# Kernel optimization log

Hardware: AMD Instinct MI355X
Metric: run time of the kernel (lower is better)

The kernel has to match this reference:

```python
import jax, jax.numpy as jnp
import numpy as np


def _gcn_conv(x, W, b, src, dst, n_nodes):
    # PyG GCNConv with add_self_loops=True, edge_weight=None (implicit ones),
    # symmetric normalization: D^{-1/2} A_hat D^{-1/2} (X W) + b
    xw = x @ W                                    # [N, H]
    loop = jnp.arange(n_nodes, dtype=src.dtype)
    src_f = jnp.concatenate([src, loop])          # [E+N]
    dst_f = jnp.concatenate([dst, loop])          # [E+N]
    w = jnp.ones(src_f.shape[0], dtype=x.dtype)
    deg = jax.ops.segment_sum(w, dst_f, num_segments=n_nodes)  # in-degree incl. self-loop
    dinv = jnp.where(deg > 0, jax.lax.rsqrt(deg), 0.0)
    norm = dinv[src_f] * dinv[dst_f]              # [E+N]
    msgs = norm[:, None] * xw[src_f]              # [E+N, H]
    out = jax.ops.segment_sum(msgs, dst_f, num_segments=n_nodes)
    return out + b


def setup_inputs() -> dict:
    key = jax.random.key(0)
    k1, k2, k3, k4 = jax.random.split(key, 4)
    N, E, D, H = 100000, 1600000, 256, 128
    x = jax.random.normal(k1, (N, D), dtype=jnp.float32)
    edge_index = jax.random.randint(k2, (2, E), 0, N, dtype=jnp.int64)
    # Glorot-scaled weights
    W1 = jax.random.normal(k3, (D, H), dtype=jnp.float32) * np.sqrt(2.0 / (D + H))
    b1 = jnp.zeros((H,), dtype=jnp.float32)
    W2 = jax.random.normal(k4, (H, 1), dtype=jnp.float32) * np.sqrt(2.0 / (H + 1))
    b2 = jnp.zeros((1,), dtype=jnp.float32)
    return {"x": x, "edge_index": edge_index, "W1": W1, "b1": b1, "W2": W2, "b2": b2}


def reference(x, edge_index, W1, b1, W2, b2):
    n_nodes = x.shape[0]
    src, dst = edge_index[0], edge_index[1]
    h = _gcn_conv(x, W1, b1, src, dst, n_nodes)   # conv1
    h = jax.nn.relu(h)                            # relu; dropout is identity in eval mode
    out = _gcn_conv(h, W2, b2, src, dst, n_nodes) # conv2 -> [N, 1]
    return out.reshape(-1)                        # x.view(-1)
```

## Files before the change

kernel.cpp:

```cpp
#include <hip/hip_runtime.h>
#include <hip/hip_fp16.h>
#include <cstdint>
#include <cstddef>


#define ELLCAP 63
#define BSH 9
#define BNODES (1 << BSH)
#define BPAD 16
#define BCAP 12288

typedef _Float16 half8 __attribute__((ext_vector_type(8)));
typedef _Float16 half2t __attribute__((ext_vector_type(2)));
typedef float floatx4 __attribute__((ext_vector_type(4)));
typedef float floatv4 __attribute__((ext_vector_type(4)));
typedef int intv4 __attribute__((ext_vector_type(4)));
typedef unsigned int uintv4 __attribute__((ext_vector_type(4)));

__global__ __launch_bounds__(256) void prep_k(const float* __restrict__ W1,
                                              _Float16* __restrict__ wz,
                                              _Float16* __restrict__ z1h,
                                              float* __restrict__ z2w,
                                              int* __restrict__ cnt,
                                              int* __restrict__ gcur,
                                              int N, int NB) {
  int b = blockIdx.x, tid = threadIdx.x;
  if (b < 128) {
    int id = b * 256 + tid;
    int j = id & 7, lane = (id >> 3) & 63, nb = (id >> 9) & 7, kb = id >> 12;
    int k = kb * 32 + ((lane >> 4) << 3) + j;
    int n = nb * 16 + (lane & 15);
    wz[id] = (_Float16)W1[k * 128 + n];
  } else if (b == 128) {
    if (tid < 128) z1h[(size_t)N * 128 + tid] = (_Float16)0.f;
    if (tid == 0) { z2w[N] = 0.f; cnt[N] = 0; }
  } else {
    int i = (b - 129) * 256 + tid;
    if (i < NB * BPAD) gcur[i] = 0;
  }
}

__global__ __launch_bounds__(256) void stage_k(int kind, int fb, int g0,
                                               const float* __restrict__ X,
                                               const _Float16* __restrict__ wz,
                                               _Float16* __restrict__ z1h, int N,
                                               const int* __restrict__ src,
                                               const int* __restrict__ dst,
                                               int* __restrict__ gcur,
                                               int* __restrict__ barr,
                                               int* __restrict__ ell,
                                               int* __restrict__ cnt,
                                               int E, int NB) {
  __shared__ char lds_raw[16 * 1024];
  int tid = threadIdx.x;

  if ((int)blockIdx.x < fb) {
    if (kind == 0) {
      int* bc = (int*)lds_raw;
      int* bb = bc + 256;
      for (int i = tid; i < NB; i += 256) bc[i] = 0;
      __syncthreads();
      int base = ((int)blockIdx.x * 256 + tid) * 8;
      int dv[8], sv[8], rv[8], bkv[8];
      int ne = 0;
      if (base + 7 < E) {
        intv4 d0 = __builtin_nontemporal_load((const intv4*)(dst + base));
        intv4 d1 = __builtin_nontemporal_load((const intv4*)(dst + base + 4));
        intv4 s0 = __builtin_nontemporal_load((const intv4*)(src + base));
        intv4 s1 = __builtin_nontemporal_load((const intv4*)(src + base + 4));
        dv[0] = d0[0]; dv[1] = d0[1]; dv[2] = d0[2]; dv[3] = d0[3];
        dv[4] = d1[0]; dv[5] = d1[1]; dv[6] = d1[2]; dv[7] = d1[3];
        sv[0] = s0[0]; sv[1] = s0[1]; sv[2] = s0[2]; sv[3] = s0[3];
        sv[4] = s1[0]; sv[5] = s1[1]; sv[6] = s1[2]; sv[7] = s1[3];
        ne = 8;
      } else {
        for (int e = base; e < E && e < base + 8; ++e) {
          dv[ne] = dst[e]; sv[ne] = src[e]; ++ne;
        }
      }
      for (int i = 0; i < ne; ++i) {
        bkv[i] = dv[i] >> BSH;
        rv[i] = atomicAdd(&bc[bkv[i]], 1);
      }
      __syncthreads();
      for (int i = tid; i < NB; i += 256) {
        int cc = bc[i];
        bb[i] = cc ? atomicAdd(&gcur[i * BPAD], cc) : 0;
      }
      __syncthreads();
      for (int i = 0; i < ne; ++i) {
        int pos = bb[bkv[i]] + rv[i];
        if (pos < BCAP) {
          unsigned dl = (unsigned)(dv[i] & (BNODES - 1));
          barr[(size_t)bkv[i] * BCAP + pos] = (int)((dl << 23) | (unsigned)sv[i]);
        }
      }
    } else {
      int* cl = (int*)lds_raw;
      int bkt = (int)blockIdx.x;
      int lo = bkt << BSH;
      for (int i = tid; i < BNODES; i += 256) cl[i] = 0;
      __syncthreads();
      int cb = min(gcur[bkt * BPAD], BCAP);
      const int* seg = barr + (size_t)bkt * BCAP;
      for (int e = tid; e < cb; e += 256) {
        unsigned v = (unsigned)seg[e];
        int dl = (int)(v >> 23);
        int s = (int)(v & 0x7FFFFFu);
        int p = atomicAdd(&cl[dl], 1);
        if (p < ELLCAP) ell[(size_t)(lo + dl) * 64 + p] = s;
      }
      __syncthreads();
      for (int i = tid; i < BNODES; i += 256) {
        int node = lo + i;
        if (node < N) cnt[node] = cl[i];
      }
    }
    return;
  }

  _Float16* Bl = (_Float16*)lds_raw;
  _Float16* Ol = (_Float16*)lds_raw;

  int wave = tid >> 6, lane = tid & 63;
  int m = lane & 15, q = lane >> 4;
  int row0 = (g0 + (int)blockIdx.x - fb) * 64;
  int row = row0 + wave * 16 + m;

  floatx4 acc[8];
#pragma unroll
  for (int nb = 0; nb < 8; ++nb) acc[nb] = (floatx4)(0.f);

  const uintv4* wsrc = (const uintv4*)wz;
  uintv4* bdst = (uintv4*)Bl;

#pragma unroll
  for (int ph = 0; ph < 4; ++ph) {
    if (ph) __syncthreads();
#pragma unroll
    for (int i = 0; i < 4; ++i) bdst[i * 256 + tid] = wsrc[ph * 1024 + i * 256 + tid];
    __syncthreads();
#pragma unroll
    for (int kk = 0; kk < 2; ++kk) {
      int kb = ph * 2 + kk;
      half8 a;
      if (row < N) {
        const floatv4* ap = (const floatv4*)(X + (size_t)row * 256 + kb * 32 + q * 8);
        floatv4 a0 = __builtin_nontemporal_load(ap);
        floatv4 a1 = __builtin_nontemporal_load(ap + 1);
        a[0] = (_Float16)a0[0]; a[1] = (_Float16)a0[1];
        a[2] = (_Float16)a0[2]; a[3] = (_Float16)a0[3];
        a[4] = (_Float16)a1[0]; a[5] = (_Float16)a1[1];
        a[6] = (_Float16)a1[2]; a[7] = (_Float16)a1[3];
      } else {
#pragma unroll
        for (int j = 0; j < 8; ++j) a[j] = (_Float16)0.f;
      }
#pragma unroll
      for (int nb = 0; nb < 8; ++nb) {
        half8 b = *(const half8*)(Bl + ((size_t)(kk * 8 + nb) * 64 + lane) * 8);
        acc[nb] = __builtin_amdgcn_mfma_f32_16x16x32_f16(a, b, acc[nb], 0, 0, 0);
      }
    }
  }
  __syncthreads();

#pragma unroll
  for (int nb = 0; nb < 8; ++nb) {
    int col = nb * 16 + m;
#pragma unroll
    for (int r = 0; r < 4; ++r) {
      int orow = wave * 16 + q * 4 + r;
      Ol[orow * 128 + col] = (_Float16)acc[nb][r];
    }
  }
  __syncthreads();

  const uintv4* osrc = (const uintv4*)Ol;
  uintv4* gdst = (uintv4*)(z1h + (size_t)row0 * 128);
#pragma unroll
  for (int i = 0; i < 4; ++i) {
    int idx = i * 256 + tid;
    int r = idx >> 4;
    if (row0 + r < N) gdst[idx] = osrc[idx];
  }
}

__global__ __launch_bounds__(256) void agg1_k(const _Float16* __restrict__ z1h,
                                              const int* __restrict__ cnt,
                                              const int* __restrict__ ell,
                                              const float* __restrict__ b1,
                                              const float* __restrict__ W2,
                                              float* __restrict__ z2w, int N) {
  int d = blockIdx.x * 4 + (threadIdx.x >> 6);
  int lane = threadIdx.x & 63;
  if (d >= N) return;
  int cd = cnt[d];
  int c = min(cd, ELLCAP);
  int ct = c + 1;
  int raw = ell[(size_t)d * 64 + lane];
  int up = __shfl_up(raw, 1, 64);
  int idx = (lane == 0) ? d : ((lane < ct) ? up : N);
  float wl = rsqrtf((float)(cnt[idx] + 1));
  float dd = rsqrtf((float)(cd + 1));

  int g = lane >> 4;
  int a8 = (lane & 15) * 8;
  float acc[8];
#pragma unroll
  for (int k = 0; k < 8; ++k) acc[k] = 0.f;

  for (int t = 0; t < ct; t += 8) {
    int s0 = __shfl(idx, t + g, 64);
    float w0 = __shfl(wl, t + g, 64);
    int s1 = __shfl(idx, t + 4 + g, 64);
    float w1 = __shfl(wl, t + 4 + g, 64);
    half8 v0 = *(const half8*)(z1h + (size_t)s0 * 128 + a8);
    half8 v1 = *(const half8*)(z1h + (size_t)s1 * 128 + a8);
#pragma unroll
    for (int k = 0; k < 8; ++k) acc[k] = fmaf(w0, (float)v0[k], acc[k]);
#pragma unroll
    for (int k = 0; k < 8; ++k) acc[k] = fmaf(w1, (float)v1[k], acc[k]);
  }

#pragma unroll
  for (int k = 0; k < 8; ++k) {
    acc[k] += __shfl_xor(acc[k], 16, 64);
    acc[k] += __shfl_xor(acc[k], 32, 64);
  }

  float4 bA = *(const float4*)(b1 + a8);
  float4 bB = *(const float4*)(b1 + a8 + 4);
  float4 wA = *(const float4*)(W2 + a8);
  float4 wB = *(const float4*)(W2 + a8 + 4);
  float dot = fmaxf(fmaf(dd, acc[0], bA.x), 0.f) * wA.x
            + fmaxf(fmaf(dd, acc[1], bA.y), 0.f) * wA.y
            + fmaxf(fmaf(dd, acc[2], bA.z), 0.f) * wA.z
            + fmaxf(fmaf(dd, acc[3], bA.w), 0.f) * wA.w
            + fmaxf(fmaf(dd, acc[4], bB.x), 0.f) * wB.x
            + fmaxf(fmaf(dd, acc[5], bB.y), 0.f) * wB.y
            + fmaxf(fmaf(dd, acc[6], bB.z), 0.f) * wB.z
            + fmaxf(fmaf(dd, acc[7], bB.w), 0.f) * wB.w;
#pragma unroll
  for (int off = 8; off >= 1; off >>= 1) dot += __shfl_xor(dot, off, 64);
  if (lane == 0) z2w[d] = dd * dot;
}

__global__ __launch_bounds__(256) void agg2_k(const float* __restrict__ z2w,
                                              const int* __restrict__ cnt,
                                              const int* __restrict__ ell,
                                              const float* __restrict__ b2,
                                              float* __restrict__ out, int N) {
  int d = blockIdx.x * 4 + (threadIdx.x >> 6);
  int lane = threadIdx.x & 63;
  if (d >= N) return;
  int cd = cnt[d];
  int c = min(cd, ELLCAP);
  int raw = ell[(size_t)d * 64 + lane];
  int idx = (lane < c) ? raw : N;
  float v = z2w[idx];
#pragma unroll
  for (int off = 32; off >= 1; off >>= 1) v += __shfl_xor(v, off, 64);
  if (lane == 0) out[d] = rsqrtf((float)(cd + 1)) * (v + z2w[d]) + b2[0];
}

extern "C" void kernel_launch(void* const* d_in, const int* in_sizes, int n_in,
                              void* d_out, int out_size, void* d_ws, size_t ws_size,
                              hipStream_t stream) {
  (void)n_in; (void)out_size; (void)ws_size;
  const float* x = (const float*)d_in[0];
  const int* edge = (const int*)d_in[1];
  const float* W1 = (const float*)d_in[2];
  const float* b1 = (const float*)d_in[3];
  const float* W2 = (const float*)d_in[4];
  const float* b2 = (const float*)d_in[5];
  float* out = (float*)d_out;

  const int D = 256, H = 128;
  int N = in_sizes[0] / D;
  int E = in_sizes[1] / 2;
  const int* srcp = edge;
  const int* dstp = edge + E;
  int NB = (N + BNODES - 1) >> BSH;

  char* ws = (char*)d_ws;
  size_t off = 0;
  auto alloc = [&](size_t bytes) -> void* {
    void* p = ws + off;
    off += (bytes + 255) & ~(size_t)255;
    return p;
  };
  int* cnt        = (int*)alloc((size_t)(N + 1) * 4);
  float* z2w      = (float*)alloc((size_t)(N + 1) * 4);
  int* ell        = (int*)alloc((size_t)N * 64 * 4);
  _Float16* wz    = (_Float16*)alloc((size_t)32768 * 2);
  _Float16* z1h   = (_Float16*)alloc((size_t)(N + 1) * H * 2);
  int* gcur       = (int*)alloc((size_t)NB * BPAD * 4);
  int* barr       = (int*)alloc((size_t)NB * BCAP * 4);

  int tiles = (N + 63) / 64;
  int fbA = (E + 2047) / 2048;
  int fbB = NB;

  prep_k<<<dim3(129 + (NB * BPAD + 255) / 256), dim3(256), 0, stream>>>(
      W1, wz, z1h, z2w, cnt, gcur, N, NB);
  stage_k<<<dim3(fbA + tiles), dim3(256), 0, stream>>>(0, fbA, 0, x, wz, z1h, N,
      srcp, dstp, gcur, barr, ell, cnt, E, NB);
  stage_k<<<dim3(fbB), dim3(256), 0, stream>>>(1, fbB, tiles, x, wz, z1h, N,
      srcp, dstp, gcur, barr, ell, cnt, E, NB);
  agg1_k<<<dim3((N + 3) / 4), dim3(256), 0, stream>>>(z1h, cnt, ell, b1, W2, z2w, N);
  agg2_k<<<dim3((N + 3) / 4), dim3(256), 0, stream>>>(z2w, cnt, ell, b2, out, N);
}
```

Baseline: 292.0 us.

## Split ELL into primary and overflow arrays, halve agg2 wave use

Stores each node's first 32 neighbours in a compact 32-wide ELL array and entries 32..62 in a separate overflow array. With an average in-degree of about 16, the gather kernels now read mostly dense 128-byte rows instead of 256-byte rows. agg2 handles two nodes per wave with 32 lanes each, and agg1 adds a 4-neighbour tail loop so it does not load padded entries. Bucket size shrinks (BSH 8, BCAP 4608) to match, which adds more buckets and more bucket-capacity pressure in the staging pass.

After: 295.2 us. No clear change (+1.1%).

```diff
diff --git a/kernel.cpp b/kernel.cpp
--- a/kernel.cpp
+++ b/kernel.cpp
@@ -4,11 +4,10 @@
 #include <cstddef>
 
 
-#define ELLCAP 63
-#define BSH 9
+#define BSH 8
 #define BNODES (1 << BSH)
 #define BPAD 16
-#define BCAP 12288
+#define BCAP 4608
 
 typedef _Float16 half8 __attribute__((ext_vector_type(8)));
 typedef _Float16 half2t __attribute__((ext_vector_type(2)));
@@ -49,6 +48,7 @@
                                                int* __restrict__ gcur,
                                                int* __restrict__ barr,
                                                int* __restrict__ ell,
+                                               int* __restrict__ ell2,
                                                int* __restrict__ cnt,
                                                int E, int NB) {
   __shared__ char lds_raw[16 * 1024];
@@ -57,7 +57,7 @@
   if ((int)blockIdx.x < fb) {
     if (kind == 0) {
       int* bc = (int*)lds_raw;
-      int* bb = bc + 256;
+      int* bb = bc + 512;
       for (int i = tid; i < NB; i += 256) bc[i] = 0;
       __syncthreads();
       int base = ((int)blockIdx.x * 256 + tid) * 8;
@@ -108,7 +108,8 @@
         int dl = (int)(v >> 23);
         int s = (int)(v & 0x7FFFFFu);
         int p = atomicAdd(&cl[dl], 1);
-        if (p < ELLCAP) ell[(size_t)(lo + dl) * 64 + p] = s;
+        if (p < 32) ell[(size_t)(lo + dl) * 32 + p] = s;
+        else if (p < 63) ell2[(size_t)(lo + dl) * 32 + (p - 32)] = s;
       }
       __syncthreads();
       for (int i = tid; i < BNODES; i += 256) {
@@ -189,6 +190,7 @@
 __global__ __launch_bounds__(256) void agg1_k(const _Float16* __restrict__ z1h,
                                               const int* __restrict__ cnt,
                                               const int* __restrict__ ell,
+                                              const int* __restrict__ ell2,
                                               const float* __restrict__ b1,
                                               const float* __restrict__ W2,
                                               float* __restrict__ z2w, int N) {
@@ -196,9 +198,15 @@
   int lane = threadIdx.x & 63;
   if (d >= N) return;
   int cd = cnt[d];
-  int c = min(cd, ELLCAP);
+  int c = min(cd, 63);
   int ct = c + 1;
-  int raw = ell[(size_t)d * 64 + lane];
+  int raw;
+  if (c > 32) {
+    raw = (lane < 32) ? ell[(size_t)d * 32 + lane]
+                      : ell2[(size_t)d * 32 + (lane - 32)];
+  } else {
+    raw = ell[(size_t)d * 32 + (lane & 31)];
+  }
   int up = __shfl_up(raw, 1, 64);
   int idx = (lane == 0) ? d : ((lane < ct) ? up : N);
   float wl = rsqrtf((float)(cnt[idx] + 1));
@@ -210,7 +218,8 @@
 #pragma unroll
   for (int k = 0; k < 8; ++k) acc[k] = 0.f;
 
-  for (int t = 0; t < ct; t += 8) {
+  int t = 0;
+  for (; t + 8 <= ct; t += 8) {
     int s0 = __shfl(idx, t + g, 64);
     float w0 = __shfl(wl, t + g, 64);
     int s1 = __shfl(idx, t + 4 + g, 64);
@@ -221,6 +230,13 @@
     for (int k = 0; k < 8; ++k) acc[k] = fmaf(w0, (float)v0[k], acc[k]);
 #pragma unroll
     for (int k = 0; k < 8; ++k) acc[k] = fmaf(w1, (float)v1[k], acc[k]);
+  }
+  for (; t < ct; t += 4) {
+    int s0 = __shfl(idx, t + g, 64);
+    float w0 = __shfl(wl, t + g, 64);
+    half8 v0 = *(const half8*)(z1h + (size_t)s0 * 128 + a8);
+#pragma unroll
+    for (int k = 0; k < 8; ++k) acc[k] = fmaf(w0, (float)v0[k], acc[k]);
   }
 
 #pragma unroll
@@ -249,19 +265,23 @@
 __global__ __launch_bounds__(256) void agg2_k(const float* __restrict__ z2w,
                                               const int* __restrict__ cnt,
                                               const int* __restrict__ ell,
+                                              const int* __restrict__ ell2,
                                               const float* __restrict__ b2,
                                               float* __restrict__ out, int N) {
-  int d = blockIdx.x * 4 + (threadIdx.x >> 6);
-  int lane = threadIdx.x & 63;
+  int wv = threadIdx.x >> 6;
+  int half = (threadIdx.x >> 5) & 1;
+  int j = threadIdx.x & 31;
+  int d = blockIdx.x * 8 + wv * 2 + half;
   if (d >= N) return;
   int cd = cnt[d];
-  int c = min(cd, ELLCAP);
-  int raw = ell[(size_t)d * 64 + lane];
-  int idx = (lane < c) ? raw : N;
+  int c = min(cd, 63);
+  int raw = ell[(size_t)d * 32 + j];
+  int idx = (j < min(c, 32)) ? raw : N;
   float v = z2w[idx];
-#pragma unroll
-  for (int off = 32; off >= 1; off >>= 1) v += __shfl_xor(v, off, 64);
-  if (lane == 0) out[d] = rsqrtf((float)(cd + 1)) * (v + z2w[d]) + b2[0];
+  if (c > 32 && j < c - 32) v += z2w[ell2[(size_t)d * 32 + j]];
+#pragma unroll
+  for (int off = 16; off >= 1; off >>= 1) v += __shfl_xor(v, off, 64);
+  if (j == 0) out[d] = rsqrtf((float)(cd + 1)) * (v + z2w[d]) + b2[0];
 }
 
 extern "C" void kernel_launch(void* const* d_in, const int* in_sizes, int n_in,
@@ -292,7 +312,8 @@
   };
   int* cnt        = (int*)alloc((size_t)(N + 1) * 4);
   float* z2w      = (float*)alloc((size_t)(N + 1) * 4);
-  int* ell        = (int*)alloc((size_t)N * 64 * 4);
+  int* ell        = (int*)alloc((size_t)N * 32 * 4);
+  int* ell2       = (int*)alloc((size_t)N * 32 * 4);
   _Float16* wz    = (_Float16*)alloc((size_t)32768 * 2);
   _Float16* z1h   = (_Float16*)alloc((size_t)(N + 1) * H * 2);
   int* gcur       = (int*)alloc((size_t)NB * BPAD * 4);
@@ -305,9 +326,9 @@
   prep_k<<<dim3(129 + (NB * BPAD + 255) / 256), dim3(256), 0, stream>>>(
       W1, wz, z1h, z2w, cnt, gcur, N, NB);
   stage_k<<<dim3(fbA + tiles), dim3(256), 0, stream>>>(0, fbA, 0, x, wz, z1h, N,
-      srcp, dstp, gcur, barr, ell, cnt, E, NB);
+      srcp, dstp, gcur, barr, ell, ell2, cnt, E, NB);
   stage_k<<<dim3(fbB), dim3(256), 0, stream>>>(1, fbB, tiles, x, wz, z1h, N,
-      srcp, dstp, gcur, barr, ell, cnt, E, NB);
-  agg1_k<<<dim3((N + 3) / 4), dim3(256), 0, stream>>>(z1h, cnt, ell, b1, W2, z2w, N);
-  agg2_k<<<dim3((N + 3) / 4), dim3(256), 0, stream>>>(z2w, cnt, ell, b2, out, N);
-}
+      srcp, dstp, gcur, barr, ell, ell2, cnt, E, NB);
+  agg1_k<<<dim3((N + 3) / 4), dim3(256), 0, stream>>>(z1h, cnt, ell, ell2, b1, W2, z2w, N);
+  agg2_k<<<dim3((N + 7) / 8), dim3(256), 0, stream>>>(z2w, cnt, ell, ell2, b2, out, N);
+}
```
